# Kernel tuning notes

Hardware: AMD Instinct MI355X
Metric: run time of the kernel (lower is better)

The kernel has to match this reference:

```python
import jax, jax.numpy as jnp
import numpy as np
from jax import lax

DN = ('NCHW', 'OIHW', 'NCHW')

def conv(x, w, b, stride, pad):
    y = lax.conv_general_dilated(x, w, (stride, stride), [(pad, pad), (pad, pad)], dimension_numbers=DN)
    return y + b[None, :, None, None]

def setup_inputs() -> dict:
    key = jax.random.key(0)
    ks = jax.random.split(key, 16)
    s = 0.05
    inp = {
        'condition': jax.random.normal(ks[0], (16, 1, 256, 256), jnp.float32),
        'w1': jax.random.normal(ks[1], (64, 1, 4, 4), jnp.float32) * s,
        'b1': jnp.zeros((64,), jnp.float32),
        'w2': jax.random.normal(ks[2], (128, 64, 4, 4), jnp.float32) * s,
        'b2': jnp.zeros((128,), jnp.float32),
        'w3': jax.random.normal(ks[3], (128, 128, 3, 3), jnp.float32) * s,
        'b3': jnp.zeros((128,), jnp.float32),
        'r1w1': jax.random.normal(ks[4], (32, 128, 3, 3), jnp.float32) * s,
        'r1b1': jnp.zeros((32,), jnp.float32),
        'r1w2': jax.random.normal(ks[5], (128, 32, 1, 1), jnp.float32) * s,
        'r1b2': jnp.zeros((128,), jnp.float32),
        'r2w1': jax.random.normal(ks[6], (32, 128, 3, 3), jnp.float32) * s,
        'r2b1': jnp.zeros((32,), jnp.float32),
        'r2w2': jax.random.normal(ks[7], (128, 32, 1, 1), jnp.float32) * s,
        'r2b2': jnp.zeros((128,), jnp.float32),
        'wpre': jax.random.normal(ks[8], (4, 128, 1, 1), jnp.float32) * s,
        'bpre': jnp.zeros((4,), jnp.float32),
        'codebook': jax.random.normal(ks[9], (2048, 4), jnp.float32),
    }
    return inp

def reference(condition, w1, b1, w2, b2, w3, b3, r1w1, r1b1, r1w2, r1b2,
              r2w1, r2b1, r2w2, r2b2, wpre, bpre, codebook):
    # --- conv encoder (VQ-VAE standard) ---
    h = jax.nn.relu(conv(condition, w1, b1, 2, 1))   # [B,64,128,128]
    h = jax.nn.relu(conv(h, w2, b2, 2, 1))           # [B,128,64,64]
    h = conv(h, w3, b3, 1, 1)                        # [B,128,64,64]
    # residual stack: 2 blocks of relu->3x3->relu->1x1, residual add
    for wa, ba, wb, bb in ((r1w1, r1b1, r1w2, r1b2), (r2w1, r2b1, r2w2, r2b2)):
        t = conv(jax.nn.relu(h), wa, ba, 1, 1)
        t = conv(jax.nn.relu(t), wb, bb, 1, 0)
        h = h + t
    h = jax.nn.relu(h)
    z = conv(h, wpre, bpre, 1, 0)                    # [B,4,64,64]
    # --- cosine-distance vector quantization ---
    B, D, H, W = z.shape
    zf = jnp.transpose(z, (0, 2, 3, 1)).reshape(-1, D)          # [BHW, D]
    zn = zf / (jnp.linalg.norm(zf, axis=-1, keepdims=True) + 1e-12)
    en = codebook / (jnp.linalg.norm(codebook, axis=-1, keepdims=True) + 1e-12)
    sim = jnp.einsum('nd,kd->nk', zn, en)                       # cosine similarity
    idx = jnp.argmax(sim, axis=-1)                              # nearest code
    q = codebook[idx].reshape(B, H, W, D)
    c = jnp.transpose(q, (0, 3, 1, 2))                          # [B,4,64,64]
    return c
```

## Files before the change

kernel.cpp:

```cpp
#include <hip/hip_runtime.h>
#include <math.h>


typedef short v8s __attribute__((ext_vector_type(8)));
typedef float v4f __attribute__((ext_vector_type(4)));

#define B_OFF 4194304
#define A_OFF 12582912
#define W2_S 0
#define W3_S 393216
#define WR1_S 835584
#define WR2_S 946176
#define WP1_S 1056768
#define WP2_S 1069056

__device__ inline void limb3(float v, unsigned short& h, unsigned short& m,
                             unsigned short& l) {
    unsigned ub = __float_as_uint(v);
    unsigned hb = ub & 0xffff0000u;
    float r1 = v - __uint_as_float(hb);
    unsigned mb = __float_as_uint(r1) & 0xffff0000u;
    float r2 = r1 - __uint_as_float(mb);
    unsigned lb = __float_as_uint(r2) & 0xffff0000u;
    h = (unsigned short)(hb >> 16);
    m = (unsigned short)(mb >> 16);
    l = (unsigned short)(lb >> 16);
}

struct CfgConv2 {
    static constexpr int NC = 8, NT = 4, OC = 128;
    static constexpr bool RELU_IN = false, RELU_OUT = true;
    __device__ static void tap(int c, int t, int& ry, int& rx) {
        int py = (c >> 2) & 1, px = (c >> 1) & 1;
        ry = (t >> 1) - py; rx = (t & 1) - px;
    }
    __device__ static bool gaddr(int n, int oy, int r, int X, int icp, int c,
                                 int& g0, int& g1) {
        int py = (c >> 2) & 1, px = (c >> 1) & 1;
        int y2 = oy + r - 1;
        if (y2 < 0 || y2 >= 64) return false;
        int pi = (c & 1) * 16 + icp;
        g0 = (((n * 4 + py * 2 + px) * 64 + y2) * 32 + pi) * 128 + X;
        g1 = g0 + 64;
        return true;
    }
    __device__ static int widx(int c, int t, int oc, int ic) {
        int py = (c >> 2) & 1, px = (c >> 1) & 1, half = c & 1;
        int dy = 2 * (t >> 1) + (1 - py), dx = 2 * (t & 1) + (1 - px);
        return ((oc * 64 + half * 32 + ic) * 4 + dy) * 4 + dx;
    }
};
struct CfgConv3 {
    static constexpr int NC = 4, NT = 9, OC = 128;
    static constexpr bool RELU_IN = false, RELU_OUT = false;
    __device__ static void tap(int c, int t, int& ry, int& rx) {
        ry = t / 3 - 1; rx = t % 3 - 1;
    }
    __device__ static bool gaddr(int n, int oy, int r, int X, int icp, int c,
                                 int& g0, int& g1) {
        int Yg = oy + r - 1;
        if (Yg < 0 || Yg >= 64) return false;
        int pi = c * 16 + icp;
        g0 = ((n * 64 + Yg) * 64 + pi) * 128 + X;
        g1 = g0 + 64;
        return true;
    }
    __device__ static int widx(int c, int t, int oc, int ic) {
        return ((oc * 128 + c * 32 + ic) * 3 + t / 3) * 3 + t % 3;
    }
};
struct CfgRes {
    static constexpr int NC = 4, NT = 9, OC = 32;
    __device__ static int widx(int c, int t, int oc, int ic) {
        return ((oc * 128 + c * 32 + ic) * 3 + t / 3) * 3 + t % 3;
    }
};
struct Cfg1x1 {
    static constexpr int NC = 1, NT = 1, OC = 128;
    __device__ static int widx(int c, int t, int oc, int ic) {
        return oc * 32 + ic;
    }
};

template <typename C>
__device__ inline void repack_one(const float* __restrict__ w,
                                  short* __restrict__ dst, int idx) {
    int s  = idx & 31;
    int oc = (idx >> 5) % C::OC;
    int ct = idx / (32 * C::OC);
    int c = ct / C::NT, t = ct % C::NT;
    float val = w[C::widx(c, t, oc, s)];
    unsigned short h, m, l;
    limb3(val, h, m, l);
    constexpr int NTILE = C::OC / 16;
    int nt = oc >> 4, o = oc & 15, q = s >> 3, j = s & 7;
    int fr = ((q * 16 + o) << 3) + j;
    dst[(((ct * 3 + 0) * NTILE + nt) << 9) + fr] = (short)h;
    dst[(((ct * 3 + 1) * NTILE + nt) << 9) + fr] = (short)m;
    dst[(((ct * 3 + 2) * NTILE + nt) << 9) + fr] = (short)l;
}

__global__ __launch_bounds__(256) void repack_all_k(
    const float* __restrict__ w2, const float* __restrict__ w3,
    const float* __restrict__ r1, const float* __restrict__ r2,
    const float* __restrict__ p1, const float* __restrict__ p2,
    short* __restrict__ base)
{
    int idx = blockIdx.x * 256 + threadIdx.x;
    if (idx < 131072) { repack_one<CfgConv2>(w2, base + W2_S, idx); return; }
    idx -= 131072;
    if (idx < 147456) { repack_one<CfgConv3>(w3, base + W3_S, idx); return; }
    idx -= 147456;
    if (idx < 36864)  { repack_one<CfgRes>(r1, base + WR1_S, idx); return; }
    idx -= 36864;
    if (idx < 36864)  { repack_one<CfgRes>(r2, base + WR2_S, idx); return; }
    idx -= 36864;
    if (idx < 4096)   { repack_one<Cfg1x1>(p1, base + WP1_S, idx); return; }
    idx -= 4096;
    if (idx < 4096)   { repack_one<Cfg1x1>(p2, base + WP2_S, idx); }
}

template <typename C>
__global__ __launch_bounds__(256, 3) void mfma_conv(
    const float* __restrict__ in, const short* __restrict__ repw,
    const float* __restrict__ bias, float* __restrict__ out, int n0)
{
    constexpr int APLANE = 3 * 66 * 32;
    constexpr int NTILE  = C::OC / 16;
    __shared__ __align__(16) short lA[3 * APLANE];

    int tid = threadIdx.x;
    int lane = tid & 63, wv = tid >> 6;
    int n_img = blockIdx.x >> 6, oy = blockIdx.x & 63;

    for (int idx = tid; idx < 3 * 3 * 2 * 16; idx += 256) {
        int plane = idx / 96;
        int rem = idx % 96;
        int rr = rem / 32;
        int hc = (rem / 16) & 1;
        int d = idx & 15;
        ((unsigned*)lA)[plane * 3168 + (rr * 66 + hc * 65) * 16 + d] = 0;
    }

    v4f acc[4][2] = {};
    int nbase = wv * 2;
    int Xq = tid & 15, icp = tid >> 4, quad = lane >> 4;

    float pv[24];
    auto issue_loads = [&](int c) {
#pragma unroll
        for (int it = 0; it < 12; it++) {
            int r = it >> 2, xg = it & 3;
            int X = xg * 16 + Xq;
            int g0, g1;
            float v0 = 0.f, v1 = 0.f;
            if (C::gaddr(n_img, oy, r, X, icp, c, g0, g1)) {
                v0 = in[g0];
                v1 = in[g1];
            }
            pv[2 * it] = v0; pv[2 * it + 1] = v1;
        }
    };
    auto load_bf = [&](int c, int t, v8s (&dst)[2][3]) {
#pragma unroll
        for (int nt = 0; nt < 2; nt++)
#pragma unroll
            for (int L = 0; L < 3; L++)
                dst[nt][L] = *(const v8s*)(repw +
                    ((((c * C::NT + t) * 3 + L) * NTILE + (nbase + nt)) << 9) +
                    (lane << 3));
    };

    issue_loads(0);

    for (int c = 0; c < C::NC; c++) {
        __syncthreads();
#pragma unroll
        for (int it = 0; it < 12; it++) {
            int r = it >> 2, xg = it & 3;
            int X = xg * 16 + Xq;
            float v0 = pv[2 * it], v1 = pv[2 * it + 1];
            if constexpr (C::RELU_IN) { v0 = fmaxf(v0, 0.f); v1 = fmaxf(v1, 0.f); }
            unsigned short h0, m0, l0, h1, m1, l1;
            limb3(v0, h0, m0, l0);
            limb3(v1, h1, m1, l1);
            int cell = r * 66 + X + 1;
            int f = (cell + (cell >> 2)) & 3;
            int phys = (icp & 3) + 4 * (((icp >> 2) + f) & 3);
            unsigned* pa = (unsigned*)lA + cell * 16 + phys;
            pa[0]        = (unsigned)h0 | ((unsigned)h1 << 16);
            pa[3168]     = (unsigned)m0 | ((unsigned)m1 << 16);
            pa[2 * 3168] = (unsigned)l0 | ((unsigned)l1 << 16);
        }
        __syncthreads();
        if (c + 1 < C::NC) issue_loads(c + 1);

        v8s bf[2][2][3];
        load_bf(c, 0, bf[0]);
#pragma unroll
        for (int t = 0; t < C::NT; t++) {
            constexpr int NTT = C::NT;
            if (t + 1 < NTT) load_bf(c, t + 1, bf[(t + 1) & 1]);
            int ry, rx;
            C::tap(c, t, ry, rx);
#pragma unroll
            for (int mt = 0; mt < 4; mt++) {
                int x = mt * 16 + (lane & 15);
                int cell = (ry + 1) * 66 + (x + rx + 1);
                int f = (cell + (cell >> 2)) & 3;
                int aa = cell * 32 + (((quad + f) & 3) << 3);
                v8s ah = *(const v8s*)&lA[aa];
                v8s am = *(const v8s*)&lA[APLANE + aa];
                v8s al = *(const v8s*)&lA[2 * APLANE + aa];
#pragma unroll
                for (int nt = 0; nt < 2; nt++) {
                    v4f a0 = acc[mt][nt];
                    a0 = __builtin_amdgcn_mfma_f32_16x16x32_bf16(ah, bf[t & 1][nt][0], a0, 0, 0, 0);
                    a0 = __builtin_amdgcn_mfma_f32_16x16x32_bf16(ah, bf[t & 1][nt][1], a0, 0, 0, 0);
                    a0 = __builtin_amdgcn_mfma_f32_16x16x32_bf16(am, bf[t & 1][nt][0], a0, 0, 0, 0);
                    a0 = __builtin_amdgcn_mfma_f32_16x16x32_bf16(am, bf[t & 1][nt][1], a0, 0, 0, 0);
                    a0 = __builtin_amdgcn_mfma_f32_16x16x32_bf16(ah, bf[t & 1][nt][2], a0, 0, 0, 0);
                    a0 = __builtin_amdgcn_mfma_f32_16x16x32_bf16(al, bf[t & 1][nt][0], a0, 0, 0, 0);
                    acc[mt][nt] = a0;
                }
            }
        }
    }
#pragma unroll
    for (int mt = 0; mt < 4; mt++) {
        int x0 = mt * 16 + quad * 4;
#pragma unroll
        for (int nt = 0; nt < 2; nt++) {
            int oc = (nbase + nt) * 16 + (lane & 15);
            float bv = bias[oc];
            float v0 = acc[mt][nt][0] + bv;
            float v1 = acc[mt][nt][1] + bv;
            float v2 = acc[mt][nt][2] + bv;
            float v3 = acc[mt][nt][3] + bv;
            if constexpr (C::RELU_OUT) {
                v0 = fmaxf(v0, 0.f); v1 = fmaxf(v1, 0.f);
                v2 = fmaxf(v2, 0.f); v3 = fmaxf(v3, 0.f);
            }
            float4 o = make_float4(v0, v1, v2, v3);
            int off = (((n0 + n_img) * 64 + oy) * 64 + (oc >> 1)) * 128 +
                      (oc & 1) * 64 + x0;
            *(float4*)&out[off] = o;
        }
    }
}

__global__ __launch_bounds__(256) void mfma_res(
    const float* __restrict__ in, const short* __restrict__ repw,
    const float* __restrict__ b1, const short* __restrict__ repp,
    const float* __restrict__ b2, float* __restrict__ out)
{
    constexpr int PLANE_D = 4 * 66 * 16;
    constexpr int PLANE_S = 2 * PLANE_D;
    __shared__ __align__(16) short lA[3 * PLANE_S];

    int tid = threadIdx.x;
    int lane = tid & 63, wv = tid >> 6;
    int n_img = blockIdx.x >> 5;
    int oy0 = (blockIdx.x & 31) << 1;
    int jrow = wv >> 1, xh = wv & 1;

    for (int idx = tid; idx < 3 * 4 * 2 * 16; idx += 256) {
        int plane = idx / 128;
        int rem = idx % 128;
        int rr = rem / 32;
        int hc = (rem >> 4) & 1;
        int d = idx & 15;
        ((unsigned*)lA)[plane * PLANE_D + (rr * 66 + hc * 65) * 16 + d] = 0;
    }

    v4f acc[2][2] = {};
    int Xq = tid & 15, icp = tid >> 4, quad = lane >> 4;

    float pv[32];
    auto issue_loads = [&](int c) {
#pragma unroll
        for (int it = 0; it < 16; it++) {
            int r = it >> 2, xg = it & 3;
            int X = xg * 16 + Xq;
            int Yg = oy0 + r - 1;
            float v0 = 0.f, v1 = 0.f;
            if (Yg >= 0 && Yg < 64) {
                int g = ((n_img * 64 + Yg) * 64 + (c * 16 + icp)) * 128 + X;
                v0 = in[g];
                v1 = in[g + 64];
            }
            pv[2 * it] = v0; pv[2 * it + 1] = v1;
        }
    };

    issue_loads(0);

    for (int c = 0; c < 4; c++) {
        __syncthreads();
#pragma unroll
        for (int it = 0; it < 16; it++) {
            int r = it >> 2, xg = it & 3;
            int X = xg * 16 + Xq;
            float v0 = fmaxf(pv[2 * it], 0.f);
            float v1 = fmaxf(pv[2 * it + 1], 0.f);
            unsigned short h0, m0, l0, h1, m1, l1;
            limb3(v0, h0, m0, l0);
            limb3(v1, h1, m1, l1);
            int cell = r * 66 + X + 1;
            int f = (cell + (cell >> 2)) & 3;
            int phys = (icp & 3) + 4 * (((icp >> 2) + f) & 3);
            unsigned* pa = (unsigned*)lA + cell * 16 + phys;
            pa[0]           = (unsigned)h0 | ((unsigned)h1 << 16);
            pa[PLANE_D]     = (unsigned)m0 | ((unsigned)m1 << 16);
            pa[2 * PLANE_D] = (unsigned)l0 | ((unsigned)l1 << 16);
        }
        __syncthreads();
        if (c + 1 < 4) issue_loads(c + 1);

        v8s bf[2][2][3];
        auto load_bf = [&](int t, v8s (&dst)[2][3]) {
#pragma unroll
            for (int nt = 0; nt < 2; nt++)
#pragma unroll
                for (int L = 0; L < 3; L++)
                    dst[nt][L] = *(const v8s*)(repw +
                        ((((c * 9 + t) * 3 + L) * 2 + nt) << 9) + (lane << 3));
        };
        load_bf(0, bf[0]);
#pragma unroll
        for (int t = 0; t < 9; t++) {
            if (t + 1 < 9) load_bf(t + 1, bf[(t + 1) & 1]);
            int ry = t / 3 - 1, rx = t % 3 - 1;
#pragma unroll
            for (int mti = 0; mti < 2; mti++) {
                int x = (xh * 2 + mti) * 16 + (lane & 15);
                int cell = (jrow + ry + 1) * 66 + (x + rx + 1);
                int f = (cell + (cell >> 2)) & 3;
                int aa = cell * 32 + (((quad + f) & 3) << 3);
                v8s ah = *(const v8s*)&lA[aa];
                v8s am = *(const v8s*)&lA[PLANE_S + aa];
                v8s al = *(const v8s*)&lA[2 * PLANE_S + aa];
#pragma unroll
                for (int nt = 0; nt < 2; nt++) {
                    v4f a0 = acc[mti][nt];
                    a0 = __builtin_amdgcn_mfma_f32_16x16x32_bf16(ah, bf[t & 1][nt][0], a0, 0, 0, 0);
                    a0 = __builtin_amdgcn_mfma_f32_16x16x32_bf16(ah, bf[t & 1][nt][1], a0, 0, 0, 0);
                    a0 = __builtin_amdgcn_mfma_f32_16x16x32_bf16(am, bf[t & 1][nt][0], a0, 0, 0, 0);
                    a0 = __builtin_amdgcn_mfma_f32_16x16x32_bf16(am, bf[t & 1][nt][1], a0, 0, 0, 0);
                    a0 = __builtin_amdgcn_mfma_f32_16x16x32_bf16(ah, bf[t & 1][nt][2], a0, 0, 0, 0);
                    a0 = __builtin_amdgcn_mfma_f32_16x16x32_bf16(al, bf[t & 1][nt][0], a0, 0, 0, 0);
                    acc[mti][nt] = a0;
                }
            }
        }
    }

    __syncthreads();
#pragma unroll
    for (int mti = 0; mti < 2; mti++) {
#pragma unroll
        for (int nt = 0; nt < 2; nt++) {
            int ic = nt * 16 + (lane & 15);
            int icp2 = ic >> 1, hilo = ic & 1;
            float bv = b1[ic];
#pragma unroll
            for (int r = 0; r < 4; r++) {
                int x = (xh * 2 + mti) * 16 + quad * 4 + r;
                float v = fmaxf(acc[mti][nt][r] + bv, 0.f);
                unsigned short h, m, l;
                limb3(v, h, m, l);
                int f = (x + (x >> 2)) & 3;
                int phys = (icp2 & 3) + 4 * (((icp2 >> 2) + f) & 3);
                int sa = x * 32 + phys * 2 + hilo;
                lA[jrow * 6144 + sa]        = (short)h;
                lA[jrow * 6144 + 2048 + sa] = (short)m;
                lA[jrow * 6144 + 4096 + sa] = (short)l;
            }
        }
    }
    __syncthreads();

#pragma unroll
    for (int j = 0; j < 2; j++) {
        v4f a2[8] = {};
        int x = wv * 16 + (lane & 15);
        int f = (x + (x >> 2)) & 3;
        int aa = x * 32 + (((quad + f) & 3) << 3);
        v8s ah = *(const v8s*)&lA[j * 6144 + aa];
        v8s am = *(const v8s*)&lA[j * 6144 + 2048 + aa];
        v8s al = *(const v8s*)&lA[j * 6144 + 4096 + aa];
#pragma unroll
        for (int nt = 0; nt < 8; nt++) {
            v8s bh = *(const v8s*)(repp + ((0 * 8 + nt) << 9) + (lane << 3));
            v8s bm = *(const v8s*)(repp + ((1 * 8 + nt) << 9) + (lane << 3));
            v8s bl = *(const v8s*)(repp + ((2 * 8 + nt) << 9) + (lane << 3));
            v4f a0 = a2[nt];
            a0 = __builtin_amdgcn_mfma_f32_16x16x32_bf16(ah, bh, a0, 0, 0, 0);
            a0 = __builtin_amdgcn_mfma_f32_16x16x32_bf16(ah, bm, a0, 0, 0, 0);
            a0 = __builtin_amdgcn_mfma_f32_16x16x32_bf16(am, bh, a0, 0, 0, 0);
            a0 = __builtin_amdgcn_mfma_f32_16x16x32_bf16(am, bm, a0, 0, 0, 0);
            a0 = __builtin_amdgcn_mfma_f32_16x16x32_bf16(ah, bl, a0, 0, 0, 0);
            a0 = __builtin_amdgcn_mfma_f32_16x16x32_bf16(al, bh, a0, 0, 0, 0);
            a2[nt] = a0;
        }
#pragma unroll
        for (int nt = 0; nt < 8; nt++) {
            int oc = nt * 16 + (lane & 15);
            int x0 = wv * 16 + quad * 4;
            int off = ((n_img * 64 + (oy0 + j)) * 64 + (oc >> 1)) * 128 +
                      (oc & 1) * 64 + x0;
            float4 hv = *(const float4*)&in[off];
            float bv = b2[oc];
            float4 o = make_float4(hv.x + a2[nt][0] + bv, hv.y + a2[nt][1] + bv,
                                   hv.z + a2[nt][2] + bv, hv.w + a2[nt][3] + bv);
            *(float4*)&out[off] = o;
        }
    }
}

__global__ __launch_bounds__(256) void conv1_k(
    const float* __restrict__ x, const float* __restrict__ w,
    const float* __restrict__ b, float* __restrict__ out)
{
    int tid = blockIdx.x * 256 + threadIdx.x;
    int n   = tid >> 14;
    int rem = tid & 16383;
    int oy  = rem >> 7;
    int ox  = rem & 127;
    int iy0 = oy * 2 - 1, ix0 = ox * 2 - 1;
    const float* xb = x + n * 65536;
    float v[16];
#pragma unroll
    for (int ky = 0; ky < 4; ky++) {
#pragma unroll
        for (int kx = 0; kx < 4; kx++) {
            int iy = iy0 + ky, ix = ix0 + kx;
            bool ok = (iy >= 0) & (iy < 256) & (ix >= 0) & (ix < 256);
            v[ky * 4 + kx] = ok ? xb[iy * 256 + ix] : 0.f;
        }
    }
    int py = oy & 1, y2 = oy >> 1, px = ox & 1, x2 = ox >> 1;
    int obase = (((n * 4 + py * 2 + px) * 64 + y2) * 32) * 128 + x2;
    for (int oc = 0; oc < 64; oc++) {
        float acc = b[oc];
        const float* wp = w + oc * 16;
#pragma unroll
        for (int k = 0; k < 16; k++) acc = fmaf(v[k], wp[k], acc);
        out[obase + (oc >> 1) * 128 + (oc & 1) * 64] = fmaxf(acc, 0.f);
    }
}

__global__ __launch_bounds__(256) void prevq_k(
    const float* __restrict__ h, const float* __restrict__ wpre,
    const float* __restrict__ bpre, const float* __restrict__ cb,
    float* __restrict__ out)
{
    __shared__ float4 en[2048];
    __shared__ float4 zpart[4][64];
    for (int i = threadIdx.x; i < 2048; i += 256) {
        float c0 = cb[i * 4 + 0], c1 = cb[i * 4 + 1];
        float c2 = cb[i * 4 + 2], c3 = cb[i * 4 + 3];
        float nrm = sqrtf(c0 * c0 + c1 * c1 + c2 * c2 + c3 * c3) + 1e-12f;
        en[i] = make_float4(c0 / nrm, c1 / nrm, c2 / nrm, c3 / nrm);
    }

    int t = threadIdx.x;
    {
        int w = t >> 6, pl = t & 63;
        int gpos = blockIdx.x * 64 + pl;
        int n = gpos >> 12, pos = gpos & 4095;
        int y = pos >> 6, xx = pos & 63;
        const float* hb = h + ((n * 64 + y) * 64) * 128 + xx;
        float z0 = 0.f, z1 = 0.f, z2 = 0.f, z3 = 0.f;
        for (int icp = w * 16; icp < w * 16 + 16; icp++) {
            float v0 = fmaxf(hb[icp * 128], 0.f);
            int ic = 2 * icp;
            z0 = fmaf(v0, wpre[ic],       z0);
            z1 = fmaf(v0, wpre[128 + ic], z1);
            z2 = fmaf(v0, wpre[256 + ic], z2);
            z3 = fmaf(v0, wpre[384 + ic], z3);
            float v1 = fmaxf(hb[icp * 128 + 64], 0.f);
            z0 = fmaf(v1, wpre[ic + 1],       z0);
            z1 = fmaf(v1, wpre[128 + ic + 1], z1);
            z2 = fmaf(v1, wpre[256 + ic + 1], z2);
            z3 = fmaf(v1, wpre[384 + ic + 1], z3);
        }
        zpart[w][pl] = make_float4(z0, z1, z2, z3);
    }
    __syncthreads();

    int part = t & 3, pl = t >> 2;
    int gpos = blockIdx.x * 64 + pl;
    int n = gpos >> 12, pos = gpos & 4095;
    float4 p0 = zpart[0][pl], p1 = zpart[1][pl];
    float4 p2 = zpart[2][pl], p3 = zpart[3][pl];
    float z0 = bpre[0] + p0.x + p1.x + p2.x + p3.x;
    float z1 = bpre[1] + p0.y + p1.y + p2.y + p3.y;
    float z2 = bpre[2] + p0.z + p1.z + p2.z + p3.z;
    float z3 = bpre[3] + p0.w + p1.w + p2.w + p3.w;

    float best = -1e30f;
    int   bidx = part * 512;
    for (int k = part * 512; k < part * 512 + 512; k++) {
        float4 e = en[k];
        float s = z0 * e.x + z1 * e.y + z2 * e.z + z3 * e.w;
        if (s > best) { best = s; bidx = k; }
    }
#pragma unroll
    for (int d = 1; d < 4; d <<= 1) {
        float ob = __shfl_xor(best, d);
        int   oi = __shfl_xor(bidx, d);
        if (ob > best || (ob == best && oi < bidx)) { best = ob; bidx = oi; }
    }
    out[(n * 4 + part) * 4096 + pos] = cb[bidx * 4 + part];
}

extern "C" void kernel_launch(void* const* d_in, const int* in_sizes, int n_in,
                              void* d_out, int out_size, void* d_ws, size_t ws_size,
                              hipStream_t stream)
{
    const float* x    = (const float*)d_in[0];
    const float* w1   = (const float*)d_in[1];
    const float* b1   = (const float*)d_in[2];
    const float* w2   = (const float*)d_in[3];
    const float* b2   = (const float*)d_in[4];
    const float* w3   = (const float*)d_in[5];
    const float* b3   = (const float*)d_in[6];
    const float* r1w1 = (const float*)d_in[7];
    const float* r1b1 = (const float*)d_in[8];
    const float* r1w2 = (const float*)d_in[9];
    const float* r1b2 = (const float*)d_in[10];
    const float* r2w1 = (const float*)d_in[11];
    const float* r2b1 = (const float*)d_in[12];
    const float* r2w2 = (const float*)d_in[13];
    const float* r2b2 = (const float*)d_in[14];
    const float* wpre = (const float*)d_in[15];
    const float* bpre = (const float*)d_in[16];
    const float* cb   = (const float*)d_in[17];
    float* out = (float*)d_out;

    float* ws   = (float*)d_ws;
    short* wsS  = (short*)d_ws;
    float* B = ws + B_OFF;
    float* A = ws + A_OFF;

    repack_all_k<<<1408, 256, 0, stream>>>(w2, w3, r1w1, r2w1, r1w2, r2w2, wsS);

    conv1_k<<<512, 256, 0, stream>>>(x,               w1, b1, A);
    mfma_conv<CfgConv2><<<512, 256, 0, stream>>>(A, wsS + W2_S, b2, B, 0);
    conv1_k<<<512, 256, 0, stream>>>(x + 8 * 65536,   w1, b1, A);
    mfma_conv<CfgConv2><<<512, 256, 0, stream>>>(A, wsS + W2_S, b2, B, 8);

    mfma_conv<CfgConv3><<<1024, 256, 0, stream>>>(B, wsS + W3_S, b3, A, 0);

    mfma_res<<<512, 256, 0, stream>>>(A, wsS + WR1_S, r1b1, wsS + WP1_S, r1b2, B);
    mfma_res<<<512, 256, 0, stream>>>(B, wsS + WR2_S, r2b1, wsS + WP2_S, r2b2, A);

    prevq_k<<<1024, 256, 0, stream>>>(A, wpre, bpre, cb, out);
}
```

Baseline: 456.6 us.

## Fuse second residual block with pre-VQ projection and codebook search

The second residual block kernel now also applies the final ReLU, the 1x1 pre-quantization projection and the cosine-distance argmax over the codebook, and writes the quantized output directly. This removes the separate prevq kernel, its 32MB intermediate write and re-read, and the per-block codebook normalization, which now runs once in the repack kernel. In exchange the codebook search reads normalized codes from global memory instead of shared memory, and the fused kernel carries more registers and a longer serial tail per block.

```diff
diff --git a/kernel.cpp b/kernel.cpp
--- a/kernel.cpp
+++ b/kernel.cpp
@@ -7,6 +7,7 @@
 
 #define B_OFF 4194304
 #define A_OFF 12582912
+#define ENCB_F 1048576
 #define W2_S 0
 #define W3_S 393216
 #define WR1_S 835584
@@ -104,7 +105,8 @@
     const float* __restrict__ w2, const float* __restrict__ w3,
     const float* __restrict__ r1, const float* __restrict__ r2,
     const float* __restrict__ p1, const float* __restrict__ p2,
-    short* __restrict__ base)
+    const float* __restrict__ cb, short* __restrict__ base,
+    float* __restrict__ encb)
 {
     int idx = blockIdx.x * 256 + threadIdx.x;
     if (idx < 131072) { repack_one<CfgConv2>(w2, base + W2_S, idx); return; }
@@ -117,7 +119,15 @@
     idx -= 36864;
     if (idx < 4096)   { repack_one<Cfg1x1>(p1, base + WP1_S, idx); return; }
     idx -= 4096;
-    if (idx < 4096)   { repack_one<Cfg1x1>(p2, base + WP2_S, idx); }
+    if (idx < 4096)   { repack_one<Cfg1x1>(p2, base + WP2_S, idx); return; }
+    idx -= 4096;
+    if (idx < 8192) {
+        int k = idx >> 2, d = idx & 3;
+        float c0 = cb[k * 4 + 0], c1 = cb[k * 4 + 1];
+        float c2 = cb[k * 4 + 2], c3 = cb[k * 4 + 3];
+        float nrm = sqrtf(c0 * c0 + c1 * c1 + c2 * c2 + c3 * c3) + 1e-12f;
+        encb[k * 4 + d] = cb[k * 4 + d] / nrm;
+    }
 }
 
 template <typename C>
@@ -418,6 +428,230 @@
     }
 }
 
+__global__ __launch_bounds__(256) void mfma_res_vq(
+    const float* __restrict__ in, const short* __restrict__ repw,
+    const float* __restrict__ b1, const short* __restrict__ repp,
+    const float* __restrict__ b2, const float* __restrict__ wpre,
+    const float* __restrict__ bpre, const float* __restrict__ encb,
+    const float* __restrict__ cb, float* __restrict__ out)
+{
+    constexpr int PLANE_D = 4 * 66 * 16;
+    constexpr int PLANE_S = 2 * PLANE_D;
+    __shared__ __align__(16) short lA[3 * PLANE_S];
+
+    int tid = threadIdx.x;
+    int lane = tid & 63, wv = tid >> 6;
+    int n_img = blockIdx.x >> 5;
+    int oy0 = (blockIdx.x & 31) << 1;
+    int jrow = wv >> 1, xh = wv & 1;
+
+    for (int idx = tid; idx < 3 * 4 * 2 * 16; idx += 256) {
+        int plane = idx / 128;
+        int rem = idx % 128;
+        int rr = rem / 32;
+        int hc = (rem >> 4) & 1;
+        int d = idx & 15;
+        ((unsigned*)lA)[plane * PLANE_D + (rr * 66 + hc * 65) * 16 + d] = 0;
+    }
+
+    v4f acc[2][2] = {};
+    int Xq = tid & 15, icp = tid >> 4, quad = lane >> 4;
+
+    float pv[32];
+    auto issue_loads = [&](int c) {
+#pragma unroll
+        for (int it = 0; it < 16; it++) {
+            int r = it >> 2, xg = it & 3;
+            int X = xg * 16 + Xq;
+            int Yg = oy0 + r - 1;
+            float v0 = 0.f, v1 = 0.f;
+            if (Yg >= 0 && Yg < 64) {
+                int g = ((n_img * 64 + Yg) * 64 + (c * 16 + icp)) * 128 + X;
+                v0 = in[g];
+                v1 = in[g + 64];
+            }
+            pv[2 * it] = v0; pv[2 * it + 1] = v1;
+        }
+    };
+
+    issue_loads(0);
+
+    for (int c = 0; c < 4; c++) {
+        __syncthreads();
+#pragma unroll
+        for (int it = 0; it < 16; it++) {
+            int r = it >> 2, xg = it & 3;
+            int X = xg * 16 + Xq;
+            float v0 = fmaxf(pv[2 * it], 0.f);
+            float v1 = fmaxf(pv[2 * it + 1], 0.f);
+            unsigned short h0, m0, l0, h1, m1, l1;
+            limb3(v0, h0, m0, l0);
+            limb3(v1, h1, m1, l1);
+            int cell = r * 66 + X + 1;
+            int f = (cell + (cell >> 2)) & 3;
+            int phys = (icp & 3) + 4 * (((icp >> 2) + f) & 3);
+            unsigned* pa = (unsigned*)lA + cell * 16 + phys;
+            pa[0]           = (unsigned)h0 | ((unsigned)h1 << 16);
+            pa[PLANE_D]     = (unsigned)m0 | ((unsigned)m1 << 16);
+            pa[2 * PLANE_D] = (unsigned)l0 | ((unsigned)l1 << 16);
+        }
+        __syncthreads();
+        if (c + 1 < 4) issue_loads(c + 1);
+
+        v8s bf[2][2][3];
+        auto load_bf = [&](int t, v8s (&dst)[2][3]) {
+#pragma unroll
+            for (int nt = 0; nt < 2; nt++)
+#pragma unroll
+                for (int L = 0; L < 3; L++)
+                    dst[nt][L] = *(const v8s*)(repw +
+                        ((((c * 9 + t) * 3 + L) * 2 + nt) << 9) + (lane << 3));
+        };
+        load_bf(0, bf[0]);
+#pragma unroll
+        for (int t = 0; t < 9; t++) {
+            if (t + 1 < 9) load_bf(t + 1, bf[(t + 1) & 1]);
+            int ry = t / 3 - 1, rx = t % 3 - 1;
+#pragma unroll
+            for (int mti = 0; mti < 2; mti++) {
+                int x = (xh * 2 + mti) * 16 + (lane & 15);
+                int cell = (jrow + ry + 1) * 66 + (x + rx + 1);
+                int f = (cell + (cell >> 2)) & 3;
+                int aa = cell * 32 + (((quad + f) & 3) << 3);
+                v8s ah = *(const v8s*)&lA[aa];
+                v8s am = *(const v8s*)&lA[PLANE_S + aa];
+                v8s al = *(const v8s*)&lA[2 * PLANE_S + aa];
+#pragma unroll
+                for (int nt = 0; nt < 2; nt++) {
+                    v4f a0 = acc[mti][nt];
+                    a0 = __builtin_amdgcn_mfma_f32_16x16x32_bf16(ah, bf[t & 1][nt][0], a0, 0, 0, 0);
+                    a0 = __builtin_amdgcn_mfma_f32_16x16x32_bf16(ah, bf[t & 1][nt][1], a0, 0, 0, 0);
+                    a0 = __builtin_amdgcn_mfma_f32_16x16x32_bf16(am, bf[t & 1][nt][0], a0, 0, 0, 0);
+                    a0 = __builtin_amdgcn_mfma_f32_16x16x32_bf16(am, bf[t & 1][nt][1], a0, 0, 0, 0);
+                    a0 = __builtin_amdgcn_mfma_f32_16x16x32_bf16(ah, bf[t & 1][nt][2], a0, 0, 0, 0);
+                    a0 = __builtin_amdgcn_mfma_f32_16x16x32_bf16(al, bf[t & 1][nt][0], a0, 0, 0, 0);
+                    acc[mti][nt] = a0;
+                }
+            }
+        }
+    }
+
+    __syncthreads();
+#pragma unroll
+    for (int mti = 0; mti < 2; mti++) {
+#pragma unroll
+        for (int nt = 0; nt < 2; nt++) {
+            int ic = nt * 16 + (lane & 15);
+            int icp2 = ic >> 1, hilo = ic & 1;
+            float bv = b1[ic];
+#pragma unroll
+            for (int r = 0; r < 4; r++) {
+                int x = (xh * 2 + mti) * 16 + quad * 4 + r;
+                float v = fmaxf(acc[mti][nt][r] + bv, 0.f);
+                unsigned short h, m, l;
+                limb3(v, h, m, l);
+                int f = (x + (x >> 2)) & 3;
+                int phys = (icp2 & 3) + 4 * (((icp2 >> 2) + f) & 3);
+                int sa = x * 32 + phys * 2 + hilo;
+                lA[jrow * 6144 + sa]        = (short)h;
+                lA[jrow * 6144 + 2048 + sa] = (short)m;
+                lA[jrow * 6144 + 4096 + sa] = (short)l;
+            }
+        }
+    }
+    __syncthreads();
+
+    float wp[8][4];
+#pragma unroll
+    for (int nt = 0; nt < 8; nt++)
+#pragma unroll
+        for (int d = 0; d < 4; d++)
+            wp[nt][d] = wpre[d * 128 + nt * 16 + (lane & 15)];
+
+#pragma unroll
+    for (int j = 0; j < 2; j++) {
+        v4f a2[8] = {};
+        int x = wv * 16 + (lane & 15);
+        int f = (x + (x >> 2)) & 3;
+        int aa = x * 32 + (((quad + f) & 3) << 3);
+        v8s ah = *(const v8s*)&lA[j * 6144 + aa];
+        v8s am = *(const v8s*)&lA[j * 6144 + 2048 + aa];
+        v8s al = *(const v8s*)&lA[j * 6144 + 4096 + aa];
+#pragma unroll
+        for (int nt = 0; nt < 8; nt++) {
+            v8s bh = *(const v8s*)(repp + ((0 * 8 + nt) << 9) + (lane << 3));
+            v8s bm = *(const v8s*)(repp + ((1 * 8 + nt) << 9) + (lane << 3));
+            v8s bl = *(const v8s*)(repp + ((2 * 8 + nt) << 9) + (lane << 3));
+            v4f a0 = a2[nt];
+            a0 = __builtin_amdgcn_mfma_f32_16x16x32_bf16(ah, bh, a0, 0, 0, 0);
+            a0 = __builtin_amdgcn_mfma_f32_16x16x32_bf16(ah, bm, a0, 0, 0, 0);
+            a0 = __builtin_amdgcn_mfma_f32_16x16x32_bf16(am, bh, a0, 0, 0, 0);
+            a0 = __builtin_amdgcn_mfma_f32_16x16x32_bf16(am, bm, a0, 0, 0, 0);
+            a0 = __builtin_amdgcn_mfma_f32_16x16x32_bf16(ah, bl, a0, 0, 0, 0);
+            a0 = __builtin_amdgcn_mfma_f32_16x16x32_bf16(al, bh, a0, 0, 0, 0);
+            a2[nt] = a0;
+        }
+        float z[4][4];
+#pragma unroll
+        for (int r = 0; r < 4; r++)
+#pragma unroll
+            for (int d = 0; d < 4; d++) z[r][d] = 0.f;
+#pragma unroll
+        for (int nt = 0; nt < 8; nt++) {
+            int oc = nt * 16 + (lane & 15);
+            int x0 = wv * 16 + quad * 4;
+            int off = ((n_img * 64 + (oy0 + j)) * 64 + (oc >> 1)) * 128 +
+                      (oc & 1) * 64 + x0;
+            float4 hv = *(const float4*)&in[off];
+            float bv = b2[oc];
+            float o0 = fmaxf(hv.x + a2[nt][0] + bv, 0.f);
+            float o1 = fmaxf(hv.y + a2[nt][1] + bv, 0.f);
+            float o2 = fmaxf(hv.z + a2[nt][2] + bv, 0.f);
+            float o3 = fmaxf(hv.w + a2[nt][3] + bv, 0.f);
+#pragma unroll
+            for (int d = 0; d < 4; d++) {
+                z[0][d] = fmaf(o0, wp[nt][d], z[0][d]);
+                z[1][d] = fmaf(o1, wp[nt][d], z[1][d]);
+                z[2][d] = fmaf(o2, wp[nt][d], z[2][d]);
+                z[3][d] = fmaf(o3, wp[nt][d], z[3][d]);
+            }
+        }
+#pragma unroll
+        for (int mask = 1; mask < 16; mask <<= 1)
+#pragma unroll
+            for (int r = 0; r < 4; r++)
+#pragma unroll
+                for (int d = 0; d < 4; d++)
+                    z[r][d] += __shfl_xor(z[r][d], mask);
+        int l15 = lane & 15;
+        int rsel = l15 >> 2, part = l15 & 3;
+        float zr0, zr1, zr2, zr3;
+        zr0 = (rsel == 0) ? z[0][0] : (rsel == 1) ? z[1][0] : (rsel == 2) ? z[2][0] : z[3][0];
+        zr1 = (rsel == 0) ? z[0][1] : (rsel == 1) ? z[1][1] : (rsel == 2) ? z[2][1] : z[3][1];
+        zr2 = (rsel == 0) ? z[0][2] : (rsel == 1) ? z[1][2] : (rsel == 2) ? z[2][2] : z[3][2];
+        zr3 = (rsel == 0) ? z[0][3] : (rsel == 1) ? z[1][3] : (rsel == 2) ? z[2][3] : z[3][3];
+        zr0 += bpre[0]; zr1 += bpre[1]; zr2 += bpre[2]; zr3 += bpre[3];
+
+        float best = -1e30f;
+        int   bidx = part * 512;
+        const float4* enb = (const float4*)encb;
+        for (int k = part * 512; k < part * 512 + 512; k++) {
+            float4 e = enb[k];
+            float s = zr0 * e.x + zr1 * e.y + zr2 * e.z + zr3 * e.w;
+            if (s > best) { best = s; bidx = k; }
+        }
+#pragma unroll
+        for (int dm = 1; dm < 4; dm <<= 1) {
+            float ob = __shfl_xor(best, dm);
+            int   oi = __shfl_xor(bidx, dm);
+            if (ob > best || (ob == best && oi < bidx)) { best = ob; bidx = oi; }
+        }
+        int posx = wv * 16 + quad * 4 + rsel;
+        int pos = (oy0 + j) * 64 + posx;
+        out[(n_img * 4 + part) * 4096 + pos] = cb[bidx * 4 + part];
+    }
+}
+
 __global__ __launch_bounds__(256) void conv1_k(
     const float* __restrict__ x, const float* __restrict__ w,
     const float* __restrict__ b, float* __restrict__ out)
@@ -448,71 +682,6 @@
         for (int k = 0; k < 16; k++) acc = fmaf(v[k], wp[k], acc);
         out[obase + (oc >> 1) * 128 + (oc & 1) * 64] = fmaxf(acc, 0.f);
     }
-}
-
-__global__ __launch_bounds__(256) void prevq_k(
-    const float* __restrict__ h, const float* __restrict__ wpre,
-    const float* __restrict__ bpre, const float* __restrict__ cb,
-    float* __restrict__ out)
-{
-    __shared__ float4 en[2048];
-    __shared__ float4 zpart[4][64];
-    for (int i = threadIdx.x; i < 2048; i += 256) {
-        float c0 = cb[i * 4 + 0], c1 = cb[i * 4 + 1];
-        float c2 = cb[i * 4 + 2], c3 = cb[i * 4 + 3];
-        float nrm = sqrtf(c0 * c0 + c1 * c1 + c2 * c2 + c3 * c3) + 1e-12f;
-        en[i] = make_float4(c0 / nrm, c1 / nrm, c2 / nrm, c3 / nrm);
-    }
-
-    int t = threadIdx.x;
-    {
-        int w = t >> 6, pl = t & 63;
-        int gpos = blockIdx.x * 64 + pl;
-        int n = gpos >> 12, pos = gpos & 4095;
-        int y = pos >> 6, xx = pos & 63;
-        const float* hb = h + ((n * 64 + y) * 64) * 128 + xx;
-        float z0 = 0.f, z1 = 0.f, z2 = 0.f, z3 = 0.f;
-        for (int icp = w * 16; icp < w * 16 + 16; icp++) {
-            float v0 = fmaxf(hb[icp * 128], 0.f);
-            int ic = 2 * icp;
-            z0 = fmaf(v0, wpre[ic],       z0);
-            z1 = fmaf(v0, wpre[128 + ic], z1);
-            z2 = fmaf(v0, wpre[256 + ic], z2);
-            z3 = fmaf(v0, wpre[384 + ic], z3);
-            float v1 = fmaxf(hb[icp * 128 + 64], 0.f);
-            z0 = fmaf(v1, wpre[ic + 1],       z0);
-            z1 = fmaf(v1, wpre[128 + ic + 1], z1);
-            z2 = fmaf(v1, wpre[256 + ic + 1], z2);
-            z3 = fmaf(v1, wpre[384 + ic + 1], z3);
-        }
-        zpart[w][pl] = make_float4(z0, z1, z2, z3);
-    }
-    __syncthreads();
-
-    int part = t & 3, pl = t >> 2;
-    int gpos = blockIdx.x * 64 + pl;
-    int n = gpos >> 12, pos = gpos & 4095;
-    float4 p0 = zpart[0][pl], p1 = zpart[1][pl];
-    float4 p2 = zpart[2][pl], p3 = zpart[3][pl];
-    float z0 = bpre[0] + p0.x + p1.x + p2.x + p3.x;
-    float z1 = bpre[1] + p0.y + p1.y + p2.y + p3.y;
-    float z2 = bpre[2] + p0.z + p1.z + p2.z + p3.z;
-    float z3 = bpre[3] + p0.w + p1.w + p2.w + p3.w;
-
-    float best = -1e30f;
-    int   bidx = part * 512;
-    for (int k = part * 512; k < part * 512 + 512; k++) {
-        float4 e = en[k];
-        float s = z0 * e.x + z1 * e.y + z2 * e.z + z3 * e.w;
-        if (s > best) { best = s; bidx = k; }
-    }
-#pragma unroll
-    for (int d = 1; d < 4; d <<= 1) {
-        float ob = __shfl_xor(best, d);
-        int   oi = __shfl_xor(bidx, d);
-        if (ob > best || (ob == best && oi < bidx)) { best = ob; bidx = oi; }
-    }
-    out[(n * 4 + part) * 4096 + pos] = cb[bidx * 4 + part];
 }
 
 extern "C" void kernel_launch(void* const* d_in, const int* in_sizes, int n_in,
@@ -541,10 +710,12 @@
 
     float* ws   = (float*)d_ws;
     short* wsS  = (short*)d_ws;
+    float* encb = ws + ENCB_F;
     float* B = ws + B_OFF;
     float* A = ws + A_OFF;
 
-    repack_all_k<<<1408, 256, 0, stream>>>(w2, w3, r1w1, r2w1, r1w2, r2w2, wsS);
+    repack_all_k<<<1440, 256, 0, stream>>>(w2, w3, r1w1, r2w1, r1w2, r2w2,
+                                           cb, wsS, encb);
 
     conv1_k<<<512, 256, 0, stream>>>(x,               w1, b1, A);
     mfma_conv<CfgConv2><<<512, 256, 0, stream>>>(A, wsS + W2_S, b2, B, 0);
@@ -554,7 +725,6 @@
     mfma_conv<CfgConv3><<<1024, 256, 0, stream>>>(B, wsS + W3_S, b3, A, 0);
 
     mfma_res<<<512, 256, 0, stream>>>(A, wsS + WR1_S, r1b1, wsS + WP1_S, r1b2, B);
-    mfma_res<<<512, 256, 0, stream>>>(B, wsS + WR2_S, r2b1, wsS + WP2_S, r2b2, A);
-
-    prevq_k<<<1024, 256, 0, stream>>>(A, wpre, bpre, cb, out);
+    mfma_res_vq<<<512, 256, 0, stream>>>(B, wsS + WR2_S, r2b1, wsS + WP2_S,
+                                         r2b2, wpre, bpre, encb, cb, out);
 }
```

After: 611.1 us. +33.8%, slower.
